# Optimization experiments

Measured on AMD Instinct MI355X. Metric: run time of the kernel, lower is better.

The kernel has to match this reference:

```python
import jax, jax.numpy as jnp
import numpy as np

QK_I2_S = 128  # weights per block; 32 packed bytes per block
RMS_EPS = 1e-6  # RMSNorm default eps (BitNetMLP builds RMSNorm without eps arg)


def unpack_simd(packed, K):
    """Unpack SIMD block-interleaved 2-bit weights to float {-1,0,1,2}-1 values.

    packed: [M, K//4] uint8. Within each 128-weight block (32 bytes):
      byte[j] bits 6:7 -> w[j+0], 4:5 -> w[j+32], 2:3 -> w[j+64], 0:1 -> w[j+96].
    """
    M = packed.shape[0]
    nb = K // QK_I2_S
    b = packed.astype(jnp.int32).reshape(M, nb, 32)
    # stack shift groups so flattened order is [j+0..31, j+32.., j+64.., j+96..]
    w = jnp.stack([(b >> 6) & 3, (b >> 4) & 3, (b >> 2) & 3, b & 3], axis=2)  # [M,nb,4,32]
    return w.reshape(M, K).astype(jnp.float32) - 1.0


def setup_inputs() -> dict:
    key = jax.random.key(0)
    ks = jax.random.split(key, 8)
    H, I = 2560, 6912
    B, S = 4, 2048
    x = jax.random.normal(ks[0], (B, S, H), dtype=jnp.float32)
    gate_packed = jax.random.randint(ks[1], (I, H // 4), 0, 256, dtype=jnp.int32).astype(jnp.uint8)
    up_packed = jax.random.randint(ks[2], (I, H // 4), 0, 256, dtype=jnp.int32).astype(jnp.uint8)
    down_packed = jax.random.randint(ks[3], (H, I // 4), 0, 256, dtype=jnp.int32).astype(jnp.uint8)
    gate_scale = jax.random.uniform(ks[4], (1,), minval=0.01, maxval=0.1, dtype=jnp.float32)
    up_scale = jax.random.uniform(ks[5], (1,), minval=0.01, maxval=0.1, dtype=jnp.float32)
    down_scale = jax.random.uniform(ks[6], (1,), minval=0.01, maxval=0.1, dtype=jnp.float32)
    norm_w = jnp.ones((I,), dtype=jnp.float32) + 0.05 * jax.random.normal(ks[7], (I,), dtype=jnp.float32)
    return {"x": x, "gate_packed": gate_packed, "gate_scale": gate_scale,
            "up_packed": up_packed, "up_scale": up_scale,
            "down_packed": down_packed, "down_scale": down_scale,
            "norm_w": norm_w}


def reference(x, gate_packed, gate_scale, up_packed, up_scale, down_packed, down_scale, norm_w):
    H = x.shape[-1]
    I = norm_w.shape[0]
    # BitLinear (fallback path math): unpack ternary weights, apply scalar weight scale
    Wg = unpack_simd(gate_packed, H) * gate_scale[0]   # [I, H]
    Wu = unpack_simd(up_packed, H) * up_scale[0]       # [I, H]
    Wd = unpack_simd(down_packed, I) * down_scale[0]   # [H, I]
    gate = jnp.einsum('bsh,ih->bsi', x, Wg)
    up = jnp.einsum('bsh,ih->bsi', x, Wu)
    hidden = jnp.square(jax.nn.relu(gate)) * up        # ReLU^2 gating
    # RMSNorm over intermediate dim
    var = jnp.mean(jnp.square(hidden), axis=-1, keepdims=True)
    hidden = norm_w * (hidden * jax.lax.rsqrt(var + RMS_EPS))
    return jnp.einsum('bsi,hi->bsh', hidden, Wd)
```

## Files before the change

kernel.cpp:

```cpp
#include <hip/hip_runtime.h>
#include <cstdint>
#include <cstddef>

#define H_DIM 2560
#define I_DIM 6912
#define NTOK  8192

typedef __attribute__((ext_vector_type(8))) __bf16 bf16x8;
typedef __attribute__((ext_vector_type(4))) float  f32x4;

__device__ inline void gld16(void* lds, const void* g) {
    __builtin_amdgcn_global_load_lds(
        (__attribute__((address_space(1))) void*)(void*)g,
        (__attribute__((address_space(3))) void*)lds, 16, 0, 0);
}

__global__ __launch_bounds__(256) void cvt_x_kernel(const float* __restrict__ x,
                                                    __bf16* __restrict__ xb, int n8) {
    int gid = blockIdx.x * 256 + threadIdx.x;
    if (gid >= n8) return;
    const float4* p = (const float4*)(x + (size_t)gid * 8);
    float4 v0 = p[0], v1 = p[1];
    bf16x8 o;
    o[0] = (__bf16)v0.x; o[1] = (__bf16)v0.y; o[2] = (__bf16)v0.z; o[3] = (__bf16)v0.w;
    o[4] = (__bf16)v1.x; o[5] = (__bf16)v1.y; o[6] = (__bf16)v1.z; o[7] = (__bf16)v1.w;
    *(bf16x8*)(xb + (size_t)gid * 8) = o;
}

__global__ __launch_bounds__(256) void unpack_gu_kernel(const int* __restrict__ gp,
                                                        const int* __restrict__ up,
                                                        __bf16* __restrict__ out) {
    const int per_row = H_DIM >> 3;
    const int half = I_DIM * per_row;
    int gid = blockIdx.x * 256 + threadIdx.x;
    if (gid >= 2 * half) return;
    const bool isup = gid >= half;
    const int g = isup ? gid - half : gid;
    const int* packed = isup ? up : gp;
    int i  = g / per_row;
    int k0 = (g % per_row) * 8;
    int blk = k0 >> 7;
    int grp = (k0 >> 5) & 3;
    int j0  = k0 & 31;
    int shift = 6 - 2 * grp;
    const int* p = packed + (size_t)i * (H_DIM >> 2) + blk * 32 + j0;
    int4 v0 = *(const int4*)p;
    int4 v1 = *(const int4*)(p + 4);
    int vals[8] = {v0.x, v0.y, v0.z, v0.w, v1.x, v1.y, v1.z, v1.w};
    bf16x8 o;
#pragma unroll
    for (int b = 0; b < 8; ++b)
        o[b] = (__bf16)(float)(((vals[b] >> shift) & 3) - 1);
    int dst = (i >> 4) * 32 + (i & 15) + (isup ? 16 : 0);
    *(bf16x8*)(out + (size_t)dst * H_DIM + k0) = o;
}

__global__ __launch_bounds__(256) void unpack_wd_kernel(const int* __restrict__ packed,
                                                        __bf16* __restrict__ out,
                                                        const float* __restrict__ norm) {
    const int per_row = I_DIM >> 3;
    int gid = blockIdx.x * 256 + threadIdx.x;
    if (gid >= H_DIM * per_row) return;
    int i  = gid / per_row;
    int k0 = (gid % per_row) * 8;
    int blk = k0 >> 7;
    int grp = (k0 >> 5) & 3;
    int j0  = k0 & 31;
    int shift = 6 - 2 * grp;
    const int* p = packed + (size_t)i * (I_DIM >> 2) + blk * 32 + j0;
    int4 v0 = *(const int4*)p;
    int4 v1 = *(const int4*)(p + 4);
    int vals[8] = {v0.x, v0.y, v0.z, v0.w, v1.x, v1.y, v1.z, v1.w};
    bf16x8 o;
#pragma unroll
    for (int b = 0; b < 8; ++b) {
        float f = (float)(((vals[b] >> shift) & 3) - 1);
        f *= norm[k0 + b];
        o[b] = (__bf16)f;
    }
    *(bf16x8*)(out + (size_t)i * I_DIM + k0) = o;
}

__global__ __launch_bounds__(256) void rms_rs_kernel(const __bf16* __restrict__ hidden,
                                                     float* __restrict__ rs) {
    const int tk = blockIdx.x;
    const __bf16* row = hidden + (size_t)tk * I_DIM;
    float s = 0.f;
    for (int idx = threadIdx.x; idx < I_DIM / 8; idx += 256) {
        bf16x8 v = *(const bf16x8*)&row[idx * 8];
#pragma unroll
        for (int j = 0; j < 8; ++j) { float f = (float)v[j]; s += f * f; }
    }
#pragma unroll
    for (int off = 32; off; off >>= 1) s += __shfl_down(s, off, 64);
    __shared__ float wsum[4];
    if ((threadIdx.x & 63) == 0) wsum[threadIdx.x >> 6] = s;
    __syncthreads();
    if (threadIdx.x == 0) {
        float tot = wsum[0] + wsum[1] + wsum[2] + wsum[3];
        rs[tk] = rsqrtf(tot / (float)I_DIM + 1e-6f);
    }
}

template<int KDIM>
__global__ __launch_bounds__(512, 2) void gemm_gu8(
    const __bf16* __restrict__ A,
    const __bf16* __restrict__ B,
    const float* __restrict__ gs_p,
    const float* __restrict__ us_p,
    __bf16* __restrict__ hidden,
    int nby)
{
    constexpr int KB = KDIM * 2;
    constexpr int NT = KDIM / 64;
    __shared__ __align__(16) char smem[131072];

    const int nwg = (int)gridDim.x;
    const int q = nwg >> 3;
    const int id = (int)blockIdx.x;
    const int wg = (id & 7) * q + (id >> 3);
    const int bx = wg / nby, by = wg % nby;
    const int m0 = bx * 256, n0 = by * 256;

    const int t = (int)threadIdx.x;
    const int lane = t & 63;
    const int wid = t >> 6;
    const int wm = wid >> 2, wn = wid & 3;
    const int l15 = lane & 15, s8 = lane >> 4;

    const int qa  = (t & 7) ^ ((t >> 3) & 7);
    const int rA2 = ((t >> 3) << 1) + (qa >> 2);
    const char* gA0 = (const char*)A + (size_t)(m0 + rA2) * KB + (qa & 3) * 16;
    const char* gA1 = (const char*)A + (size_t)(m0 + 128 + rA2) * KB + (qa & 3) * 16;
    const int sr0 = t >> 3, sr1 = 64 + (t >> 3);
    const int br0 = ((sr0 >> 5) << 6) + (sr0 & 31);
    const int br1 = ((sr1 >> 5) << 6) + (sr1 & 31);
    const char* gB0 = (const char*)B + (size_t)(n0 + br0) * KB + qa * 16;
    const char* gB1 = (const char*)B + (size_t)(n0 + br1) * KB + qa * 16;
    char* ldst = smem + t * 16;

    const int aoff = (wm * 64 + (l15 >> 1)) * 128 +
                     (((((l15 & 1) << 2) | s8) ^ ((l15 >> 1) & 7)) << 4);
    const int boff = (wn * 32 + l15) * 128;
    const int bco0 = ((s8) ^ (l15 & 7)) << 4;
    const int bco1 = ((4 | s8) ^ (l15 & 7)) << 4;

    f32x4 acc[8][4];
#pragma unroll
    for (int f = 0; f < 8; ++f)
#pragma unroll
        for (int n = 0; n < 4; ++n) acc[f][n] = (f32x4){0, 0, 0, 0};

#define STG_A(d, kt, kk) do {                                              \
        size_t _oA = (size_t)(kt) * 128 + (kk) * 64;                       \
        gld16(ldst + (d) * 65536 + (kk) * 16384,        gA0 + _oA);        \
        gld16(ldst + (d) * 65536 + (kk) * 16384 + 8192, gA1 + _oA);        \
    } while (0)
#define STG_B(d, kt, nh) do {                                              \
        size_t _oB = (size_t)(nh) * 32 * KB + (size_t)(kt) * 128;          \
        gld16(ldst + (d) * 65536 + 32768 + (nh) * 16384,        gB0 + _oB);\
        gld16(ldst + (d) * 65536 + 32768 + (nh) * 16384 + 8192, gB1 + _oB);\
    } while (0)
#define LOAD_A(d, kk) do { _Pragma("unroll")                               \
        for (int _f = 0; _f < 8; ++_f)                                     \
            a[_f] = *(const bf16x8*)(smem + (d) * 65536 + (kk) * 16384 +   \
                                     _f * 1024 + aoff); } while (0)
#define LOAD_B(d, nh) do {                                                 \
        b0 = *(const bf16x8*)(smem + (d) * 65536 + 32768 + (nh) * 16384 +  \
                              boff + bcur);                                \
        b1 = *(const bf16x8*)(smem + (d) * 65536 + 32768 + (nh) * 16384 +  \
                              boff + bcur + 2048); } while (0)
#define MFMA16(nh) do { __builtin_amdgcn_s_setprio(1); _Pragma("unroll")   \
        for (int _f = 0; _f < 8; ++_f) {                                   \
            acc[_f][(nh) * 2] = __builtin_amdgcn_mfma_f32_16x16x32_bf16(   \
                a[_f], b0, acc[_f][(nh) * 2], 0, 0, 0);                    \
            acc[_f][(nh) * 2 + 1] = __builtin_amdgcn_mfma_f32_16x16x32_bf16(\
                a[_f], b1, acc[_f][(nh) * 2 + 1], 0, 0, 0); }              \
        __builtin_amdgcn_s_setprio(0); } while (0)
#define BAR() do { asm volatile("" ::: "memory");                          \
        __builtin_amdgcn_s_barrier();                                      \
        asm volatile("" ::: "memory"); } while (0)
#define WAITK() do { asm volatile("s_waitcnt lgkmcnt(0)" ::: "memory");    \
        __builtin_amdgcn_sched_barrier(0); } while (0)

    STG_A(0, 0, 0); STG_A(0, 0, 1); STG_B(0, 0, 0); STG_B(0, 0, 1);
    STG_A(1, 1, 0); STG_B(1, 1, 0);
    asm volatile("s_waitcnt vmcnt(4)" ::: "memory");
    BAR();

    bf16x8 a[8], b0, b1;
    for (int kt = 0; kt < NT; ++kt) {
        const int d = kt & 1;
        int bcur = bco0;
        LOAD_A(d, 0); LOAD_B(d, 0);
        if (kt + 1 < NT) STG_A(d ^ 1, kt + 1, 1);
        BAR(); WAITK(); MFMA16(0); BAR();
        LOAD_B(d, 1);
        if (kt + 1 < NT) STG_B(d ^ 1, kt + 1, 1);
        BAR(); WAITK(); MFMA16(1); BAR();
        bcur = bco1;
        LOAD_A(d, 1); LOAD_B(d, 0);
        if (kt + 2 < NT) STG_A(d, kt + 2, 0);
        BAR(); WAITK(); MFMA16(0); BAR();
        LOAD_B(d, 1);
        if (kt + 2 < NT) {
            STG_B(d, kt + 2, 0);
            asm volatile("s_waitcnt vmcnt(4)" ::: "memory");
        } else {
            asm volatile("s_waitcnt vmcnt(0)" ::: "memory");
        }
        BAR(); WAITK(); MFMA16(1); BAR();
    }

#undef STG_A
#undef STG_B
#undef LOAD_A
#undef LOAD_B
#undef MFMA16
#undef BAR
#undef WAITK

    const float comb = gs_p[0] * gs_p[0] * us_p[0];
    const int r0 = m0 + wm * 128 + s8 * 4;
#pragma unroll
    for (int f = 0; f < 8; ++f)
#pragma unroll
        for (int p = 0; p < 2; ++p)
#pragma unroll
            for (int j = 0; j < 4; ++j) {
                float g = acc[f][2 * p][j];
                float u = acc[f][2 * p + 1][j];
                float r = fmaxf(g, 0.f);
                hidden[(size_t)(r0 + f * 16 + j) * I_DIM +
                       ((by * 8 + wn * 2 + p) * 16 + l15)] = (__bf16)(comb * r * r * u);
            }
}

template<int KDIM>
__global__ __launch_bounds__(512) void gemm_down_pipe(
    const __bf16* __restrict__ A,
    const __bf16* __restrict__ B,
    const float* __restrict__ ds_p,
    const float* __restrict__ rs,
    float* __restrict__ outf,
    int nby)
{
    constexpr int BM = 256, BN = 128, BK = 64;
    constexpr int NT = KDIM / BK;
    constexpr int SLOTB = (BM + BN) * BK * 2;
    __shared__ __align__(16) char smem[3 * SLOTB];

    const int nwg = (int)gridDim.x;
    const int q = nwg >> 3;
    const int id = (int)blockIdx.x;
    const int wg = (id & 7) * q + (id >> 3);
    const int bx = wg / nby;
    const int by = wg % nby;

    const int m0 = bx * BM;
    const int n0 = by * BN;
    const int t  = (int)threadIdx.x;
    const int lane = t & 63;
    const int wm = (t >> 6) >> 1;
    const int wn = (t >> 6) & 1;

    const int srow = t >> 3;
    const int scol = ((t & 7) * 16) ^ ((srow & 7) << 4);
    const char* gA = (const char*)A + (size_t)(m0 + srow) * (KDIM * 2) + scol;
    const char* gB = (const char*)B + (size_t)(n0 + srow) * (KDIM * 2) + scol;
    char* lbase = smem + t * 16;

    const int l15 = lane & 15;
    const int xv  = (l15 & 7) << 4;
    const int colx[2] = { (((lane >> 4) * 16) ^ xv), ((64 + (lane >> 4) * 16) ^ xv) };

    f32x4 acc[4][4];
#pragma unroll
    for (int a = 0; a < 4; ++a)
#pragma unroll
        for (int b = 0; b < 4; ++b) acc[a][b] = (f32x4){0, 0, 0, 0};

#define STAGE_T(s, kt) do {                                                     \
        char* _ls = lbase + (s) * SLOTB;                                        \
        const char* _ga = gA + (kt) * (BK * 2);                                 \
        _Pragma("unroll")                                                       \
        for (int _i = 0; _i < 4; ++_i)                                          \
            gld16(_ls + _i * 8192, _ga + (size_t)_i * 64 * (KDIM * 2));         \
        const char* _gb = gB + (kt) * (BK * 2);                                 \
        char* _lb = _ls + BM * BK * 2;                                          \
        _Pragma("unroll")                                                       \
        for (int _i = 0; _i < 2; ++_i)                                          \
            gld16(_lb + _i * 8192, _gb + (size_t)_i * 64 * (KDIM * 2));         \
    } while (0)

#define COMPUTE_T(s) do {                                                       \
        const char* _sa = smem + (s) * SLOTB;                                   \
        const char* _sb = _sa + BM * BK * 2;                                    \
        _Pragma("unroll")                                                       \
        for (int _kk = 0; _kk < 2; ++_kk) {                                     \
            bf16x8 _a[4], _b[4];                                                \
            _Pragma("unroll")                                                   \
            for (int _f = 0; _f < 4; ++_f)                                      \
                _a[_f] = *(const bf16x8*)(_sa + (wm * 64 + _f * 16 + l15) * 128 + colx[_kk]); \
            _Pragma("unroll")                                                   \
            for (int _f = 0; _f < 4; ++_f)                                      \
                _b[_f] = *(const bf16x8*)(_sb + (wn * 64 + _f * 16 + l15) * 128 + colx[_kk]); \
            __builtin_amdgcn_s_setprio(1);                                      \
            _Pragma("unroll")                                                   \
            for (int _fm = 0; _fm < 4; ++_fm)                                   \
                _Pragma("unroll")                                               \
                for (int _fn = 0; _fn < 4; ++_fn)                               \
                    acc[_fm][_fn] = __builtin_amdgcn_mfma_f32_16x16x32_bf16(    \
                        _a[_fm], _b[_fn], acc[_fm][_fn], 0, 0, 0);              \
            __builtin_amdgcn_s_setprio(0);                                      \
        }                                                                       \
    } while (0)

    STAGE_T(0, 0);
    STAGE_T(1, 1);
    asm volatile("s_waitcnt vmcnt(6)" ::: "memory");
    __builtin_amdgcn_s_barrier();
    asm volatile("" ::: "memory");

    for (int kt = 0; kt < NT; ++kt) {
        if (kt + 2 < NT) STAGE_T((kt + 2) % 3, kt + 2);
        COMPUTE_T(kt % 3);
        if (kt + 2 < NT) {
            asm volatile("s_waitcnt vmcnt(6)" ::: "memory");
            __builtin_amdgcn_s_barrier();
            asm volatile("" ::: "memory");
        } else if (kt + 2 == NT) {
            asm volatile("s_waitcnt vmcnt(0)" ::: "memory");
            __builtin_amdgcn_s_barrier();
            asm volatile("" ::: "memory");
        }
    }

#undef STAGE_T
#undef COMPUTE_T

    const float ds = ds_p[0];
    const int r0 = m0 + wm * 64 + (lane >> 4) * 4;
#pragma unroll
    for (int fm = 0; fm < 4; ++fm)
#pragma unroll
        for (int j = 0; j < 4; ++j) {
            const int row = r0 + fm * 16 + j;
            const float sc = ds * rs[row];
#pragma unroll
            for (int fn = 0; fn < 4; ++fn)
                outf[(size_t)row * H_DIM + (n0 + wn * 64 + fn * 16 + l15)] =
                    sc * acc[fm][fn][j];
        }
}

extern "C" void kernel_launch(void* const* d_in, const int* in_sizes, int n_in,
                              void* d_out, int out_size, void* d_ws, size_t ws_size,
                              hipStream_t stream) {
    const float* x   = (const float*)d_in[0];
    const int*   gp  = (const int*)d_in[1];
    const float* gs  = (const float*)d_in[2];
    const int*   upk = (const int*)d_in[3];
    const float* us  = (const float*)d_in[4];
    const int*   dp  = (const int*)d_in[5];
    const float* dsc = (const float*)d_in[6];
    const float* nw  = (const float*)d_in[7];
    float* out = (float*)d_out;

    char* ws = (char*)d_ws;
    __bf16* xb     = (__bf16*)ws;  ws += (size_t)NTOK * H_DIM * 2;
    __bf16* bgu    = (__bf16*)ws;  ws += (size_t)2 * I_DIM * H_DIM * 2;
    __bf16* wdb    = (__bf16*)ws;  ws += (size_t)H_DIM * I_DIM * 2;
    __bf16* hidden = (__bf16*)ws;  ws += (size_t)NTOK * I_DIM * 2;
    float*  rsbuf  = (float*)ws;   ws += (size_t)NTOK * 4;

    cvt_x_kernel<<<(NTOK * H_DIM / 8 + 255) / 256, 256, 0, stream>>>(x, xb, NTOK * H_DIM / 8);
    unpack_gu_kernel<<<(2 * I_DIM * H_DIM / 8 + 255) / 256, 256, 0, stream>>>(gp, upk, bgu);
    unpack_wd_kernel<<<(H_DIM * I_DIM / 8 + 255) / 256, 256, 0, stream>>>(dp, wdb, nw);

    gemm_gu8<H_DIM><<<dim3((NTOK / 256) * (2 * I_DIM / 256)), 512, 0, stream>>>(
        xb, bgu, gs, us, hidden, 2 * I_DIM / 256);

    rms_rs_kernel<<<NTOK, 256, 0, stream>>>(hidden, rsbuf);

    gemm_down_pipe<I_DIM><<<dim3((NTOK / 256) * (H_DIM / 128)), 512, 0, stream>>>(
        hidden, wdb, dsc, rsbuf, out, H_DIM / 128);
}
```

Measured before the change: 826.5 us.

## Fuse RMS sum-of-squares into gate/up epilogue, merge prep kernels, trim barriers

```diff
diff --git a/kernel.cpp b/kernel.cpp
--- a/kernel.cpp
+++ b/kernel.cpp
@@ -15,90 +15,63 @@
         (__attribute__((address_space(3))) void*)lds, 16, 0, 0);
 }
 
-__global__ __launch_bounds__(256) void cvt_x_kernel(const float* __restrict__ x,
-                                                    __bf16* __restrict__ xb, int n8) {
-    int gid = blockIdx.x * 256 + threadIdx.x;
-    if (gid >= n8) return;
-    const float4* p = (const float4*)(x + (size_t)gid * 8);
-    float4 v0 = p[0], v1 = p[1];
-    bf16x8 o;
-    o[0] = (__bf16)v0.x; o[1] = (__bf16)v0.y; o[2] = (__bf16)v0.z; o[3] = (__bf16)v0.w;
-    o[4] = (__bf16)v1.x; o[5] = (__bf16)v1.y; o[6] = (__bf16)v1.z; o[7] = (__bf16)v1.w;
-    *(bf16x8*)(xb + (size_t)gid * 8) = o;
-}
-
-__global__ __launch_bounds__(256) void unpack_gu_kernel(const int* __restrict__ gp,
-                                                        const int* __restrict__ up,
-                                                        __bf16* __restrict__ out) {
-    const int per_row = H_DIM >> 3;
-    const int half = I_DIM * per_row;
-    int gid = blockIdx.x * 256 + threadIdx.x;
-    if (gid >= 2 * half) return;
-    const bool isup = gid >= half;
-    const int g = isup ? gid - half : gid;
-    const int* packed = isup ? up : gp;
-    int i  = g / per_row;
-    int k0 = (g % per_row) * 8;
-    int blk = k0 >> 7;
-    int grp = (k0 >> 5) & 3;
-    int j0  = k0 & 31;
-    int shift = 6 - 2 * grp;
-    const int* p = packed + (size_t)i * (H_DIM >> 2) + blk * 32 + j0;
-    int4 v0 = *(const int4*)p;
-    int4 v1 = *(const int4*)(p + 4);
-    int vals[8] = {v0.x, v0.y, v0.z, v0.w, v1.x, v1.y, v1.z, v1.w};
-    bf16x8 o;
-#pragma unroll
-    for (int b = 0; b < 8; ++b)
-        o[b] = (__bf16)(float)(((vals[b] >> shift) & 3) - 1);
-    int dst = (i >> 4) * 32 + (i & 15) + (isup ? 16 : 0);
-    *(bf16x8*)(out + (size_t)dst * H_DIM + k0) = o;
-}
-
-__global__ __launch_bounds__(256) void unpack_wd_kernel(const int* __restrict__ packed,
-                                                        __bf16* __restrict__ out,
-                                                        const float* __restrict__ norm) {
-    const int per_row = I_DIM >> 3;
-    int gid = blockIdx.x * 256 + threadIdx.x;
-    if (gid >= H_DIM * per_row) return;
-    int i  = gid / per_row;
-    int k0 = (gid % per_row) * 8;
-    int blk = k0 >> 7;
-    int grp = (k0 >> 5) & 3;
-    int j0  = k0 & 31;
-    int shift = 6 - 2 * grp;
-    const int* p = packed + (size_t)i * (I_DIM >> 2) + blk * 32 + j0;
-    int4 v0 = *(const int4*)p;
-    int4 v1 = *(const int4*)(p + 4);
-    int vals[8] = {v0.x, v0.y, v0.z, v0.w, v1.x, v1.y, v1.z, v1.w};
-    bf16x8 o;
-#pragma unroll
-    for (int b = 0; b < 8; ++b) {
-        float f = (float)(((vals[b] >> shift) & 3) - 1);
-        f *= norm[k0 + b];
-        o[b] = (__bf16)f;
-    }
-    *(bf16x8*)(out + (size_t)i * I_DIM + k0) = o;
-}
-
-__global__ __launch_bounds__(256) void rms_rs_kernel(const __bf16* __restrict__ hidden,
-                                                     float* __restrict__ rs) {
-    const int tk = blockIdx.x;
-    const __bf16* row = hidden + (size_t)tk * I_DIM;
-    float s = 0.f;
-    for (int idx = threadIdx.x; idx < I_DIM / 8; idx += 256) {
-        bf16x8 v = *(const bf16x8*)&row[idx * 8];
-#pragma unroll
-        for (int j = 0; j < 8; ++j) { float f = (float)v[j]; s += f * f; }
-    }
-#pragma unroll
-    for (int off = 32; off; off >>= 1) s += __shfl_down(s, off, 64);
-    __shared__ float wsum[4];
-    if ((threadIdx.x & 63) == 0) wsum[threadIdx.x >> 6] = s;
-    __syncthreads();
-    if (threadIdx.x == 0) {
-        float tot = wsum[0] + wsum[1] + wsum[2] + wsum[3];
-        rs[tk] = rsqrtf(tot / (float)I_DIM + 1e-6f);
+#define NB_CVT 10240
+#define NB_GU  17280
+#define NB_WD  8640
+
+__global__ __launch_bounds__(256) void prep_kernel(
+    const float* __restrict__ x, __bf16* __restrict__ xb,
+    const int* __restrict__ gp, const int* __restrict__ up, __bf16* __restrict__ bgu,
+    const int* __restrict__ dp, const float* __restrict__ nw, __bf16* __restrict__ wdb)
+{
+    const int bid = blockIdx.x;
+    if (bid < NB_CVT) {
+        int gid = bid * 256 + threadIdx.x;
+        const float4* p = (const float4*)(x + (size_t)gid * 8);
+        float4 v0 = p[0], v1 = p[1];
+        bf16x8 o;
+        o[0] = (__bf16)v0.x; o[1] = (__bf16)v0.y; o[2] = (__bf16)v0.z; o[3] = (__bf16)v0.w;
+        o[4] = (__bf16)v1.x; o[5] = (__bf16)v1.y; o[6] = (__bf16)v1.z; o[7] = (__bf16)v1.w;
+        *(bf16x8*)(xb + (size_t)gid * 8) = o;
+    } else if (bid < NB_CVT + NB_GU) {
+        const int per_row = H_DIM >> 3;
+        const int half = I_DIM * per_row;
+        int gid = (bid - NB_CVT) * 256 + threadIdx.x;
+        const bool isup = gid >= half;
+        const int g = isup ? gid - half : gid;
+        const int* packed = isup ? up : gp;
+        int i  = g / per_row;
+        int k0 = (g % per_row) * 8;
+        int blk = k0 >> 7, grp = (k0 >> 5) & 3, j0 = k0 & 31;
+        int shift = 6 - 2 * grp;
+        const int* p = packed + (size_t)i * (H_DIM >> 2) + blk * 32 + j0;
+        int4 v0 = *(const int4*)p;
+        int4 v1 = *(const int4*)(p + 4);
+        int vals[8] = {v0.x, v0.y, v0.z, v0.w, v1.x, v1.y, v1.z, v1.w};
+        bf16x8 o;
+#pragma unroll
+        for (int b = 0; b < 8; ++b)
+            o[b] = (__bf16)(float)(((vals[b] >> shift) & 3) - 1);
+        int dst = (i >> 4) * 32 + (i & 15) + (isup ? 16 : 0);
+        *(bf16x8*)(bgu + (size_t)dst * H_DIM + k0) = o;
+    } else {
+        const int per_row = I_DIM >> 3;
+        int gid = (bid - NB_CVT - NB_GU) * 256 + threadIdx.x;
+        int i  = gid / per_row;
+        int k0 = (gid % per_row) * 8;
+        int blk = k0 >> 7, grp = (k0 >> 5) & 3, j0 = k0 & 31;
+        int shift = 6 - 2 * grp;
+        const int* p = dp + (size_t)i * (I_DIM >> 2) + blk * 32 + j0;
+        int4 v0 = *(const int4*)p;
+        int4 v1 = *(const int4*)(p + 4);
+        int vals[8] = {v0.x, v0.y, v0.z, v0.w, v1.x, v1.y, v1.z, v1.w};
+        bf16x8 o;
+#pragma unroll
+        for (int b = 0; b < 8; ++b) {
+            float f = (float)(((vals[b] >> shift) & 3) - 1);
+            o[b] = (__bf16)(f * nw[k0 + b]);
+        }
+        *(bf16x8*)(wdb + (size_t)i * I_DIM + k0) = o;
     }
 }
 
@@ -109,6 +82,7 @@
     const float* __restrict__ gs_p,
     const float* __restrict__ us_p,
     __bf16* __restrict__ hidden,
+    float* rsbuf,
     int nby)
 {
     constexpr int KB = KDIM * 2;
@@ -194,14 +168,14 @@
         int bcur = bco0;
         LOAD_A(d, 0); LOAD_B(d, 0);
         if (kt + 1 < NT) STG_A(d ^ 1, kt + 1, 1);
-        BAR(); WAITK(); MFMA16(0); BAR();
+        WAITK(); MFMA16(0); BAR();
         LOAD_B(d, 1);
         if (kt + 1 < NT) STG_B(d ^ 1, kt + 1, 1);
-        BAR(); WAITK(); MFMA16(1); BAR();
+        WAITK(); MFMA16(1); BAR();
         bcur = bco1;
         LOAD_A(d, 1); LOAD_B(d, 0);
         if (kt + 2 < NT) STG_A(d, kt + 2, 0);
-        BAR(); WAITK(); MFMA16(0); BAR();
+        WAITK(); MFMA16(0); BAR();
         LOAD_B(d, 1);
         if (kt + 2 < NT) {
             STG_B(d, kt + 2, 0);
@@ -209,7 +183,7 @@
         } else {
             asm volatile("s_waitcnt vmcnt(0)" ::: "memory");
         }
-        BAR(); WAITK(); MFMA16(1); BAR();
+        WAITK(); MFMA16(1); BAR();
     }
 
 #undef STG_A
@@ -225,15 +199,24 @@
 #pragma unroll
     for (int f = 0; f < 8; ++f)
 #pragma unroll
-        for (int p = 0; p < 2; ++p)
-#pragma unroll
-            for (int j = 0; j < 4; ++j) {
+        for (int j = 0; j < 4; ++j) {
+            float ssum = 0.f;
+#pragma unroll
+            for (int p = 0; p < 2; ++p) {
                 float g = acc[f][2 * p][j];
                 float u = acc[f][2 * p + 1][j];
                 float r = fmaxf(g, 0.f);
+                float h = comb * r * r * u;
                 hidden[(size_t)(r0 + f * 16 + j) * I_DIM +
-                       ((by * 8 + wn * 2 + p) * 16 + l15)] = (__bf16)(comb * r * r * u);
+                       ((by * 8 + wn * 2 + p) * 16 + l15)] = (__bf16)h;
+                ssum += h * h;
             }
+            ssum += __shfl_xor(ssum, 1, 64);
+            ssum += __shfl_xor(ssum, 2, 64);
+            ssum += __shfl_xor(ssum, 4, 64);
+            ssum += __shfl_xor(ssum, 8, 64);
+            if (l15 == 0) atomicAdd(&rsbuf[r0 + f * 16 + j], ssum);
+        }
 }
 
 template<int KDIM>
@@ -346,7 +329,7 @@
 #pragma unroll
         for (int j = 0; j < 4; ++j) {
             const int row = r0 + fm * 16 + j;
-            const float sc = ds * rs[row];
+            const float sc = ds * rsqrtf(rs[row] * (1.f / I_DIM) + 1e-6f);
 #pragma unroll
             for (int fn = 0; fn < 4; ++fn)
                 outf[(size_t)row * H_DIM + (n0 + wn * 64 + fn * 16 + l15)] =
@@ -374,14 +357,13 @@
     __bf16* hidden = (__bf16*)ws;  ws += (size_t)NTOK * I_DIM * 2;
     float*  rsbuf  = (float*)ws;   ws += (size_t)NTOK * 4;
 
-    cvt_x_kernel<<<(NTOK * H_DIM / 8 + 255) / 256, 256, 0, stream>>>(x, xb, NTOK * H_DIM / 8);
-    unpack_gu_kernel<<<(2 * I_DIM * H_DIM / 8 + 255) / 256, 256, 0, stream>>>(gp, upk, bgu);
-    unpack_wd_kernel<<<(H_DIM * I_DIM / 8 + 255) / 256, 256, 0, stream>>>(dp, wdb, nw);
+    hipMemsetAsync(rsbuf, 0, (size_t)NTOK * 4, stream);
+
+    prep_kernel<<<NB_CVT + NB_GU + NB_WD, 256, 0, stream>>>(
+        x, xb, gp, upk, bgu, dp, nw, wdb);
 
     gemm_gu8<H_DIM><<<dim3((NTOK / 256) * (2 * I_DIM / 256)), 512, 0, stream>>>(
-        xb, bgu, gs, us, hidden, 2 * I_DIM / 256);
-
-    rms_rs_kernel<<<NTOK, 256, 0, stream>>>(hidden, rsbuf);
+        xb, bgu, gs, us, hidden, rsbuf, 2 * I_DIM / 256);
 
     gemm_down_pipe<I_DIM><<<dim3((NTOK / 256) * (H_DIM / 128)), 512, 0, stream>>>(
         hidden, wdb, dsc, rsbuf, out, H_DIM / 128);
```

After: 857.0 us. +3.7%, slower.
